# Kernel tuning notes

Hardware: AMD Instinct MI355X
Metric: run time of the kernel (lower is better)

## Reference

```python
import jax, jax.numpy as jnp
import numpy as np

EPS = 1e-5

def _quant_w(w):
    # symmetric per-tensor 8-bit weight quantization with straight-through estimator
    s = jnp.max(jnp.abs(w)) / 127.0
    wq = jnp.round(jnp.clip(w / s, -127.0, 127.0)) * s
    return w + jax.lax.stop_gradient(wq - w)

def _adder_conv(x, w, stride):
    # AdderNet conv: out[b,co,ow] = -sum_{cin,k} |x[b,cin,ow*stride+k] - w[co,cin,k]|
    # x: (B, Cin, L), w: (Co, Cin, K)
    B, Cin, L = x.shape
    Co, _, K = w.shape
    Ow = (L - K) // stride + 1
    idx = jnp.arange(Ow)[:, None] * stride + jnp.arange(K)[None, :]      # (Ow, K)
    patches = x[:, :, idx]                                               # (B, Cin, Ow, K)
    diff = jnp.abs(patches[:, None] - w[None, :, :, None, :])            # (B, Co, Cin, Ow, K)
    return -diff.sum(axis=(2, 4))                                        # (B, Co, Ow)

def _bn(x, p):
    # eval-mode BatchNorm; x: (B,C,W), p: (4,C) = [gamma, beta, running_mean, running_var]
    g, b, m, v = p
    return (x - m[:, None]) * (g[:, None] * jax.lax.rsqrt(v[:, None] + EPS)) + b[:, None]

def _bn_params(key, c):
    k1, k2, k3, k4 = jax.random.split(key, 4)
    g = jax.random.uniform(k1, (c,)) + 0.5
    b = 0.1 * jax.random.normal(k2, (c,))
    m = 0.1 * jax.random.normal(k3, (c,))
    v = jax.random.uniform(k4, (c,)) + 0.5
    return jnp.stack([g, b, m, v]).astype(jnp.float32)

def setup_inputs() -> dict:
    key = jax.random.key(0)
    ks = jax.random.split(key, 22)
    B = 8192
    w = lambda k, shp: (0.1 * jax.random.normal(k, shp)).astype(jnp.float32)
    return {
        'x': jax.random.normal(ks[0], (B, 1, 1, 256), dtype=jnp.float32),
        'w_pre1': w(ks[1], (5, 1, 13)),   'bn_pre1': _bn_params(ks[2], 5),
        'w_pre2': w(ks[3], (10, 5, 9)),   'bn_pre2': _bn_params(ks[4], 10),
        'w_r1':   w(ks[5], (10, 10, 1)),  'bn_r1':   _bn_params(ks[6], 10),
        'w_r2':   w(ks[7], (10, 10, 1)),  'bn_r2':   _bn_params(ks[8], 10),
        'w_o1a':  w(ks[9], (70, 140, 1)), 'bn_o1a':  _bn_params(ks[10], 70),
        'w_o1b':  w(ks[11], (30, 70, 1)), 'bn_o1b':  _bn_params(ks[12], 30),
        'w_o1c':  w(ks[13], (1, 30, 1)),  'bn_o1c':  _bn_params(ks[14], 1),
        'w_o2a':  w(ks[15], (70, 140, 1)),'bn_o2a':  _bn_params(ks[16], 70),
        'w_o2b':  w(ks[17], (30, 70, 1)), 'bn_o2b':  _bn_params(ks[18], 30),
        'w_o2c':  w(ks[19], (1, 30, 1)),  'bn_o2c':  _bn_params(ks[20], 1),
    }

def reference(x, w_pre1, bn_pre1, w_pre2, bn_pre2, w_r1, bn_r1, w_r2, bn_r2,
              w_o1a, bn_o1a, w_o1b, bn_o1b, w_o1c, bn_o1c,
              w_o2a, bn_o2a, w_o2b, bn_o2b, w_o2c, bn_o2c):
    relu = jax.nn.relu
    B = x.shape[0]
    h = x.reshape(B, 1, 256)                                  # height dim is 1 -> 1D
    h = relu(_bn(_adder_conv(h, _quant_w(w_pre1), 5), bn_pre1))   # (B,5,49)
    h = relu(_bn(_adder_conv(h, _quant_w(w_pre2), 3), bn_pre2))   # (B,10,14)
    # ResBlock
    t = relu(_bn(_adder_conv(h, _quant_w(w_r1), 1), bn_r1))
    t = _bn(_adder_conv(t, _quant_w(w_r2), 1), bn_r2)
    h = relu(t + h)                                           # (B,10,14)
    f = h.reshape(B, 140, 1)                                  # flatten to channels
    # O1 branch (amplitude-weighted average lifetime)
    a = relu(_bn(_adder_conv(f, _quant_w(w_o1a), 1), bn_o1a))
    a = relu(_bn(_adder_conv(a, _quant_w(w_o1b), 1), bn_o1b))
    a = relu(_bn(_adder_conv(a, _quant_w(w_o1c), 1), bn_o1c))
    tau_amp = a.reshape(-1)                                   # (B,)
    # O2 branch (intensity-weighted average lifetime)
    b = relu(_bn(_adder_conv(f, _quant_w(w_o2a), 1), bn_o2a))
    b = relu(_bn(_adder_conv(b, _quant_w(w_o2b), 1), bn_o2b))
    b = relu(_bn(_adder_conv(b, _quant_w(w_o2c), 1), bn_o2c))
    tau_inten = b.reshape(-1)                                 # (B,)
    return (tau_amp, tau_inten)
```

## Files before the change

### kernel.cpp

```cpp
#include <hip/hip_runtime.h>

#define TPB 256
#define EPB 8
#define H1S 246
#define ES  280

#define WQ1   0
#define WQ2   65
#define WR1Q  515
#define WR2Q  615
#define WCQ   715
#define WSB   779
#define SMALL_N 1253
#define WQAT  1280
#define WQBT  20880

#define SB_P1 0
#define SB_P2 10
#define SB_R1 30
#define SB_R2 50
#define SB_A1 70
#define SB_B1 210
#define SB_C1 270
#define SB_A2 272
#define SB_B2 412
#define SB_C2 472

#define GFOLD(bn, C, OFF)                                                     \
  if (tid < (C)) {                                                            \
    float gg = (bn)[tid], bb = (bn)[(C) + tid];                               \
    float mm = (bn)[2 * (C) + tid], vv = (bn)[3 * (C) + tid];                 \
    float sc = gg / sqrtf(vv + 1e-5f);                                        \
    sbp[(OFF) + tid] = sc;                                                    \
    sbp[(OFF) + (C) + tid] = bb - mm * sc;                                    \
  }

extern "C" __global__ __launch_bounds__(256)
void prep(const float* __restrict__ w1,  const float* __restrict__ bnp1,
          const float* __restrict__ w2,  const float* __restrict__ bnp2,
          const float* __restrict__ wr1, const float* __restrict__ bnr1,
          const float* __restrict__ wr2, const float* __restrict__ bnr2,
          const float* __restrict__ wa1, const float* __restrict__ bna1,
          const float* __restrict__ wb1, const float* __restrict__ bnb1,
          const float* __restrict__ wc1, const float* __restrict__ bnc1,
          const float* __restrict__ wa2, const float* __restrict__ bna2,
          const float* __restrict__ wb2, const float* __restrict__ bnb2,
          const float* __restrict__ wc2, const float* __restrict__ bnc2,
          float* __restrict__ ws)
{
  __shared__ float s_red[4];
  const int tid = threadIdx.x;
  const int b = blockIdx.x;

  if (b == 10) {
    float* sbp = ws + WSB;
    GFOLD(bnp1, 5, SB_P1)  GFOLD(bnp2, 10, SB_P2)
    GFOLD(bnr1, 10, SB_R1) GFOLD(bnr2, 10, SB_R2)
    GFOLD(bna1, 70, SB_A1) GFOLD(bnb1, 30, SB_B1) GFOLD(bnc1, 1, SB_C1)
    GFOLD(bna2, 70, SB_A2) GFOLD(bnb2, 30, SB_B2) GFOLD(bnc2, 1, SB_C2)
    return;
  }

  const float* src; int n; int mode; int rofs; float* dst = ws;
  int ofs = 0;
  switch (b) {
    case 0: src = w1;  ofs = WQ1;      n = 65;   mode = 0; rofs = 0;  break;
    case 1: src = w2;  ofs = WQ2;      n = 450;  mode = 0; rofs = 0;  break;
    case 2: src = wr1; ofs = WR1Q;     n = 100;  mode = 0; rofs = 0;  break;
    case 3: src = wr2; ofs = WR2Q;     n = 100;  mode = 0; rofs = 0;  break;
    case 4: src = wa1; ofs = WQAT;     n = 9800; mode = 1; rofs = 0;  break;
    case 5: src = wb1; ofs = WQBT;     n = 2100; mode = 2; rofs = 0;  break;
    case 6: src = wc1; ofs = WCQ;      n = 30;   mode = 0; rofs = 0;  break;
    case 7: src = wa2; ofs = WQAT;     n = 9800; mode = 1; rofs = 70; break;
    case 8: src = wb2; ofs = WQBT;     n = 2100; mode = 2; rofs = 30; break;
    default:src = wc2; ofs = WCQ + 32; n = 30;   mode = 0; rofs = 0;  break;
  }

  float m = 0.f;
  for (int i = tid; i < n; i += 256) m = fmaxf(m, fabsf(src[i]));
#pragma unroll
  for (int off = 32; off > 0; off >>= 1)
    m = fmaxf(m, __shfl_down(m, off, 64));
  if ((tid & 63) == 0) s_red[tid >> 6] = m;
  __syncthreads();
  m = fmaxf(fmaxf(s_red[0], s_red[1]), fmaxf(s_red[2], s_red[3]));

  float s = m / 127.0f;
  for (int i = tid; i < n; i += 256) {
    float w = src[i];
    float q = rintf(fminf(fmaxf(w / s, -127.f), 127.f)) * s;
    if (mode == 0) {
      dst[ofs + i] = q;
    } else if (mode == 1) {
      int r = i / 140 + rofs, c = i % 140;
      dst[ofs + ((c >> 2) * 140 + r) * 4 + (c & 3)] = q;
    } else {
      int r = i / 70 + rofs, c = i % 70;
      dst[ofs + ((c >> 1) * 60 + r) * 2 + (c & 1)] = q;
    }
  }
}

extern "C" __global__ __launch_bounds__(TPB, 4)
void taunet(const float* __restrict__ x, const float* __restrict__ ws,
            float* __restrict__ out, int B)
{
  __shared__ __align__(16) float s_h1[EPB * H1S];
  __shared__ __align__(16) float s_e[EPB * ES];
  __shared__ __align__(16) float s_small[SMALL_N];

  const int tid = threadIdx.x;
  const int g  = tid >> 5;
  const int l  = tid & 31;
  const int ln = tid & 63;
  const int wv = tid >> 6;
  const int gp = 2 * wv;
  const int elem = blockIdx.x * EPB + g;

  for (int i = WCQ + ln; i < SMALL_N; i += 64) s_small[i] = ws[i];

  {
    const float4* xb = (const float4*)x;
#pragma unroll
    for (int it = 0; it < 2; ++it) {
      int e = gp + it;
      int ge = blockIdx.x * EPB + e;
      if (ge < B) {
        float4 v = xb[ge * 64 + ln];
        *(float4*)&s_e[e * ES + ln * 4] = v;
      }
    }
  }

  {
    const float* xe = &s_e[g * ES];
#pragma unroll
    for (int rep = 0; rep < 2; ++rep) {
      int p = l + 32 * rep;
      bool act = p < 49;
      int ps = act ? p : 0;
      float win[13];
#pragma unroll
      for (int k = 0; k < 13; ++k) win[k] = xe[5 * ps + k];
#pragma unroll
      for (int ci = 0; ci < 5; ++ci) {
        float a0 = 0.f, a1 = 0.f;
#pragma unroll
        for (int k = 0; k < 13; ++k) {
          float d = fabsf(win[k] - ws[WQ1 + ci * 13 + k]);
          if (k & 1) a1 += d; else a0 += d;
        }
        float v = fmaxf(fmaf(-(a0 + a1), ws[WSB + SB_P1 + ci],
                             ws[WSB + SB_P1 + 5 + ci]), 0.f);
        if (act) s_h1[g * H1S + ci * 49 + ps] = v;
      }
    }
  }

  float h2r[10];
  {
    const bool act = l < 14;
    const int ow = act ? l : 0;
    const float* h1b = &s_h1[g * H1S];
    float acc[10] = {0.f,0.f,0.f,0.f,0.f,0.f,0.f,0.f,0.f,0.f};
#pragma unroll
    for (int ci = 0; ci < 5; ++ci) {
      float w9[9];
#pragma unroll
      for (int k = 0; k < 9; ++k) w9[k] = h1b[ci * 49 + 3 * ow + k];
#pragma unroll
      for (int co = 0; co < 10; ++co) {
        float s0 = 0.f, s1 = 0.f;
#pragma unroll
        for (int k = 0; k < 9; ++k) {
          float d = fabsf(w9[k] - ws[WQ2 + co * 45 + ci * 9 + k]);
          if (k & 1) s1 += d; else s0 += d;
        }
        acc[co] += s0 + s1;
      }
    }
#pragma unroll
    for (int co = 0; co < 10; ++co)
      h2r[co] = fmaxf(fmaf(-acc[co], ws[WSB + SB_P2 + co],
                           ws[WSB + SB_P2 + 10 + co]), 0.f);
  }

  float t1r[10];
#pragma unroll
  for (int co = 0; co < 10; ++co) {
    float a0 = 0.f, a1 = 0.f;
#pragma unroll
    for (int ci = 0; ci < 10; ++ci) {
      float d = fabsf(h2r[ci] - ws[WR1Q + co * 10 + ci]);
      if (ci & 1) a1 += d; else a0 += d;
    }
    t1r[co] = fmaxf(fmaf(-(a0 + a1), ws[WSB + SB_R1 + co],
                         ws[WSB + SB_R1 + 10 + co]), 0.f);
  }

#pragma unroll
  for (int co = 0; co < 10; ++co) {
    float a0 = 0.f, a1 = 0.f;
#pragma unroll
    for (int ci = 0; ci < 10; ++ci) {
      float d = fabsf(t1r[ci] - ws[WR2Q + co * 10 + ci]);
      if (ci & 1) a1 += d; else a0 += d;
    }
    float t2 = fmaf(-(a0 + a1), ws[WSB + SB_R2 + co], ws[WSB + SB_R2 + 10 + co]);
    float h = fmaxf(t2 + h2r[co], 0.f);
    if (l < 14) s_e[g * ES + co * 14 + l] = h;
  }

  {
    const float* hb0 = &s_e[gp * ES];
    const float* hb1 = &s_e[(gp + 1) * ES];

    const int r2 = (ln + 128 > 139) ? 139 : ln + 128;
    float accA[3][4], accB[3][4];
#pragma unroll
    for (int p = 0; p < 3; ++p)
#pragma unroll
      for (int j = 0; j < 4; ++j) { accA[p][j] = 0.f; accB[p][j] = 0.f; }
    const int rows[3] = {ln, ln + 64, r2};
#pragma unroll 2
    for (int cb = 0; cb < 35; ++cb) {
      float4 h4 = *(const float4*)&hb0[cb * 4];
      float4 k4 = *(const float4*)&hb1[cb * 4];
#pragma unroll
      for (int p = 0; p < 3; ++p) {
        float4 w4 = *(const float4*)&ws[WQAT + (cb * 140 + rows[p]) * 4];
        accA[p][0] += fabsf(h4.x - w4.x);
        accA[p][1] += fabsf(h4.y - w4.y);
        accA[p][2] += fabsf(h4.z - w4.z);
        accA[p][3] += fabsf(h4.w - w4.w);
        accB[p][0] += fabsf(k4.x - w4.x);
        accB[p][1] += fabsf(k4.y - w4.y);
        accB[p][2] += fabsf(k4.z - w4.z);
        accB[p][3] += fabsf(k4.w - w4.w);
      }
    }
#pragma unroll
    for (int p = 0; p < 3; ++p) {
      int cl = rows[p];
      bool act = (p < 2) || (ln < 12);
      if (act) {
        int co  = cl < 70 ? cl : cl - 70;
        int off = cl < 70 ? SB_A1 : SB_A2;
        float sc = s_small[WSB + off + co], bi = s_small[WSB + off + 70 + co];
        float sadA = (accA[p][0] + accA[p][1]) + (accA[p][2] + accA[p][3]);
        float sadB = (accB[p][0] + accB[p][1]) + (accB[p][2] + accB[p][3]);
        s_h1[gp * H1S + cl]       = fmaxf(fmaf(-sadA, sc, bi), 0.f);
        s_h1[(gp + 1) * H1S + cl] = fmaxf(fmaf(-sadB, sc, bi), 0.f);
      }
    }

    {
      bool act = ln < 60;
      int rl = act ? ln : 0;
      int br = rl >= 30;
      int co = br ? rl - 30 : rl;
      const float* h0 = &s_h1[gp * H1S + br * 70];
      const float* h1 = &s_h1[(gp + 1) * H1S + br * 70];
      int off = br ? SB_B2 : SB_B1;
      float a0 = 0.f, a1 = 0.f, b0 = 0.f, b1 = 0.f;
#pragma unroll 8
      for (int ci = 0; ci < 35; ++ci) {
        float2 w2v = *(const float2*)&ws[WQBT + (ci * 60 + rl) * 2];
        a0 += fabsf(h0[2 * ci]     - w2v.x);
        a1 += fabsf(h0[2 * ci + 1] - w2v.y);
        b0 += fabsf(h1[2 * ci]     - w2v.x);
        b1 += fabsf(h1[2 * ci + 1] - w2v.y);
      }
      if (act) {
        float sc = s_small[WSB + off + co], bi = s_small[WSB + off + 30 + co];
        s_e[gp * ES + 140 + rl]       = fmaxf(fmaf(-(a0 + a1), sc, bi), 0.f);
        s_e[(gp + 1) * ES + 140 + rl] = fmaxf(fmaf(-(b0 + b1), sc, bi), 0.f);
      }
    }

    for (int br = 0; br < 2; ++br) {
      float d = 0.f;
      if (l < 30)
        d = fabsf(s_e[g * ES + 140 + br * 30 + l] - s_small[WCQ + br * 32 + l]);
#pragma unroll
      for (int off = 16; off > 0; off >>= 1)
        d += __shfl_down(d, off, 32);
      if (l == 0 && elem < B) {
        int sbC = br ? SB_C2 : SB_C1;
        out[br * B + elem] =
            fmaxf(fmaf(-d, ws[WSB + sbC], ws[WSB + sbC + 1]), 0.f);
      }
    }
  }
}

extern "C" void kernel_launch(void* const* d_in, const int* in_sizes, int n_in,
                              void* d_out, int out_size, void* d_ws, size_t ws_size,
                              hipStream_t stream) {
  const float* x    = (const float*)d_in[0];
  const float* w1   = (const float*)d_in[1];
  const float* bnp1 = (const float*)d_in[2];
  const float* w2   = (const float*)d_in[3];
  const float* bnp2 = (const float*)d_in[4];
  const float* wr1  = (const float*)d_in[5];
  const float* bnr1 = (const float*)d_in[6];
  const float* wr2  = (const float*)d_in[7];
  const float* bnr2 = (const float*)d_in[8];
  const float* wa1  = (const float*)d_in[9];
  const float* bna1 = (const float*)d_in[10];
  const float* wb1  = (const float*)d_in[11];
  const float* bnb1 = (const float*)d_in[12];
  const float* wc1  = (const float*)d_in[13];
  const float* bnc1 = (const float*)d_in[14];
  const float* wa2  = (const float*)d_in[15];
  const float* bna2 = (const float*)d_in[16];
  const float* wb2  = (const float*)d_in[17];
  const float* bnb2 = (const float*)d_in[18];
  const float* wc2  = (const float*)d_in[19];
  const float* bnc2 = (const float*)d_in[20];

  float* ws = (float*)d_ws;
  int B = in_sizes[0] / 256;
  int blocks = (B + EPB - 1) / EPB;

  hipLaunchKernelGGL(prep, dim3(11), dim3(256), 0, stream,
                     w1, bnp1, w2, bnp2, wr1, bnr1, wr2, bnr2,
                     wa1, bna1, wb1, bnb1, wc1, bnc1,
                     wa2, bna2, wb2, bnb2, wc2, bnc2, ws);

  hipLaunchKernelGGL(taunet, dim3(blocks), dim3(TPB), 0, stream,
                     x, ws, (float*)d_out, B);
}
```

Measured before the change: 146.3 us.

## Process four elements per wavefront to reuse weight loads across more samples

The block now handles 16 samples instead of 8, and each 64-lane wavefront owns 4 samples instead of 2. The 140->70 and 70->30 adder layers reuse each global weight load across four samples rather than two, and the first layers are remapped to full 64-lane wavefronts. This aims to halve weight-load traffic per sample and cut grid size, at the cost of higher register use (48 accumulators) and more shared memory per block, which may reduce occupancy.

Result: no change. 148.4 us (+1.4%).

```diff
diff --git a/kernel.cpp b/kernel.cpp
--- a/kernel.cpp
+++ b/kernel.cpp
@@ -1,7 +1,7 @@
 #include <hip/hip_runtime.h>
 
 #define TPB 256
-#define EPB 8
+#define EPB 16
 #define H1S 246
 #define ES  280
 
@@ -110,58 +110,56 @@
   __shared__ __align__(16) float s_small[SMALL_N];
 
   const int tid = threadIdx.x;
-  const int g  = tid >> 5;
-  const int l  = tid & 31;
-  const int ln = tid & 63;
+  const int l  = tid & 63;
   const int wv = tid >> 6;
-  const int gp = 2 * wv;
-  const int elem = blockIdx.x * EPB + g;
-
-  for (int i = WCQ + ln; i < SMALL_N; i += 64) s_small[i] = ws[i];
+  const int gp = 4 * wv;
+  const int ebase = blockIdx.x * EPB + gp;
+
+  for (int i = WCQ + l; i < SMALL_N; i += 64) s_small[i] = ws[i];
 
   {
     const float4* xb = (const float4*)x;
 #pragma unroll
-    for (int it = 0; it < 2; ++it) {
-      int e = gp + it;
-      int ge = blockIdx.x * EPB + e;
+    for (int j = 0; j < 4; ++j) {
+      int ge = ebase + j;
       if (ge < B) {
-        float4 v = xb[ge * 64 + ln];
-        *(float4*)&s_e[e * ES + ln * 4] = v;
-      }
-    }
-  }
-
-  {
-    const float* xe = &s_e[g * ES];
-#pragma unroll
-    for (int rep = 0; rep < 2; ++rep) {
-      int p = l + 32 * rep;
-      bool act = p < 49;
-      int ps = act ? p : 0;
-      float win[13];
-#pragma unroll
-      for (int k = 0; k < 13; ++k) win[k] = xe[5 * ps + k];
-#pragma unroll
-      for (int ci = 0; ci < 5; ++ci) {
-        float a0 = 0.f, a1 = 0.f;
-#pragma unroll
-        for (int k = 0; k < 13; ++k) {
-          float d = fabsf(win[k] - ws[WQ1 + ci * 13 + k]);
-          if (k & 1) a1 += d; else a0 += d;
-        }
-        float v = fmaxf(fmaf(-(a0 + a1), ws[WSB + SB_P1 + ci],
-                             ws[WSB + SB_P1 + 5 + ci]), 0.f);
-        if (act) s_h1[g * H1S + ci * 49 + ps] = v;
-      }
-    }
-  }
+        float4 v = xb[ge * 64 + l];
+        *(float4*)&s_e[(gp + j) * ES + l * 4] = v;
+      }
+    }
+  }
+
+#pragma unroll
+  for (int j = 0; j < 4; ++j) {
+    const float* xe = &s_e[(gp + j) * ES];
+    bool act = l < 49;
+    int ps = act ? l : 0;
+    float win[13];
+#pragma unroll
+    for (int k = 0; k < 13; ++k) win[k] = xe[5 * ps + k];
+#pragma unroll
+    for (int ci = 0; ci < 5; ++ci) {
+      float a0 = 0.f, a1 = 0.f;
+#pragma unroll
+      for (int k = 0; k < 13; ++k) {
+        float d = fabsf(win[k] - ws[WQ1 + ci * 13 + k]);
+        if (k & 1) a1 += d; else a0 += d;
+      }
+      float v = fmaxf(fmaf(-(a0 + a1), ws[WSB + SB_P1 + ci],
+                           ws[WSB + SB_P1 + 5 + ci]), 0.f);
+      if (act) s_h1[(gp + j) * H1S + ci * 49 + ps] = v;
+    }
+  }
+
+  const int eloc = l >> 4;
+  const int slot = gp + eloc;
+  const int ow16 = l & 15;
+  const bool act = ow16 < 14;
+  const int ow = act ? ow16 : 0;
 
   float h2r[10];
   {
-    const bool act = l < 14;
-    const int ow = act ? l : 0;
-    const float* h1b = &s_h1[g * H1S];
+    const float* h1b = &s_h1[slot * H1S];
     float acc[10] = {0.f,0.f,0.f,0.f,0.f,0.f,0.f,0.f,0.f,0.f};
 #pragma unroll
     for (int ci = 0; ci < 5; ++ci) {
@@ -208,88 +206,97 @@
     }
     float t2 = fmaf(-(a0 + a1), ws[WSB + SB_R2 + co], ws[WSB + SB_R2 + 10 + co]);
     float h = fmaxf(t2 + h2r[co], 0.f);
-    if (l < 14) s_e[g * ES + co * 14 + l] = h;
+    if (act) s_e[slot * ES + co * 14 + ow] = h;
   }
 
   {
-    const float* hb0 = &s_e[gp * ES];
-    const float* hb1 = &s_e[(gp + 1) * ES];
-
-    const int r2 = (ln + 128 > 139) ? 139 : ln + 128;
-    float accA[3][4], accB[3][4];
+    const int r2 = (l + 128 > 139) ? 139 : l + 128;
+    const int rows[3] = {l, l + 64, r2};
+    float acc[3][4][4];
 #pragma unroll
     for (int p = 0; p < 3; ++p)
 #pragma unroll
-      for (int j = 0; j < 4; ++j) { accA[p][j] = 0.f; accB[p][j] = 0.f; }
-    const int rows[3] = {ln, ln + 64, r2};
-#pragma unroll 2
+      for (int e = 0; e < 4; ++e)
+#pragma unroll
+        for (int c = 0; c < 4; ++c) acc[p][e][c] = 0.f;
+#pragma unroll 1
     for (int cb = 0; cb < 35; ++cb) {
-      float4 h4 = *(const float4*)&hb0[cb * 4];
-      float4 k4 = *(const float4*)&hb1[cb * 4];
+      float4 h4[4];
+#pragma unroll
+      for (int e = 0; e < 4; ++e)
+        h4[e] = *(const float4*)&s_e[(gp + e) * ES + cb * 4];
 #pragma unroll
       for (int p = 0; p < 3; ++p) {
         float4 w4 = *(const float4*)&ws[WQAT + (cb * 140 + rows[p]) * 4];
-        accA[p][0] += fabsf(h4.x - w4.x);
-        accA[p][1] += fabsf(h4.y - w4.y);
-        accA[p][2] += fabsf(h4.z - w4.z);
-        accA[p][3] += fabsf(h4.w - w4.w);
-        accB[p][0] += fabsf(k4.x - w4.x);
-        accB[p][1] += fabsf(k4.y - w4.y);
-        accB[p][2] += fabsf(k4.z - w4.z);
-        accB[p][3] += fabsf(k4.w - w4.w);
+#pragma unroll
+        for (int e = 0; e < 4; ++e) {
+          acc[p][e][0] += fabsf(h4[e].x - w4.x);
+          acc[p][e][1] += fabsf(h4[e].y - w4.y);
+          acc[p][e][2] += fabsf(h4[e].z - w4.z);
+          acc[p][e][3] += fabsf(h4[e].w - w4.w);
+        }
       }
     }
 #pragma unroll
     for (int p = 0; p < 3; ++p) {
       int cl = rows[p];
-      bool act = (p < 2) || (ln < 12);
-      if (act) {
+      bool pact = (p < 2) || (l < 12);
+      if (pact) {
         int co  = cl < 70 ? cl : cl - 70;
         int off = cl < 70 ? SB_A1 : SB_A2;
         float sc = s_small[WSB + off + co], bi = s_small[WSB + off + 70 + co];
-        float sadA = (accA[p][0] + accA[p][1]) + (accA[p][2] + accA[p][3]);
-        float sadB = (accB[p][0] + accB[p][1]) + (accB[p][2] + accB[p][3]);
-        s_h1[gp * H1S + cl]       = fmaxf(fmaf(-sadA, sc, bi), 0.f);
-        s_h1[(gp + 1) * H1S + cl] = fmaxf(fmaf(-sadB, sc, bi), 0.f);
-      }
-    }
-
-    {
-      bool act = ln < 60;
-      int rl = act ? ln : 0;
-      int br = rl >= 30;
-      int co = br ? rl - 30 : rl;
-      const float* h0 = &s_h1[gp * H1S + br * 70];
-      const float* h1 = &s_h1[(gp + 1) * H1S + br * 70];
-      int off = br ? SB_B2 : SB_B1;
-      float a0 = 0.f, a1 = 0.f, b0 = 0.f, b1 = 0.f;
-#pragma unroll 8
-      for (int ci = 0; ci < 35; ++ci) {
-        float2 w2v = *(const float2*)&ws[WQBT + (ci * 60 + rl) * 2];
-        a0 += fabsf(h0[2 * ci]     - w2v.x);
-        a1 += fabsf(h0[2 * ci + 1] - w2v.y);
-        b0 += fabsf(h1[2 * ci]     - w2v.x);
-        b1 += fabsf(h1[2 * ci + 1] - w2v.y);
-      }
-      if (act) {
-        float sc = s_small[WSB + off + co], bi = s_small[WSB + off + 30 + co];
-        s_e[gp * ES + 140 + rl]       = fmaxf(fmaf(-(a0 + a1), sc, bi), 0.f);
-        s_e[(gp + 1) * ES + 140 + rl] = fmaxf(fmaf(-(b0 + b1), sc, bi), 0.f);
-      }
-    }
-
-    for (int br = 0; br < 2; ++br) {
-      float d = 0.f;
-      if (l < 30)
-        d = fabsf(s_e[g * ES + 140 + br * 30 + l] - s_small[WCQ + br * 32 + l]);
-#pragma unroll
-      for (int off = 16; off > 0; off >>= 1)
-        d += __shfl_down(d, off, 32);
-      if (l == 0 && elem < B) {
-        int sbC = br ? SB_C2 : SB_C1;
-        out[br * B + elem] =
-            fmaxf(fmaf(-d, ws[WSB + sbC], ws[WSB + sbC + 1]), 0.f);
-      }
+#pragma unroll
+        for (int e = 0; e < 4; ++e) {
+          float sad = (acc[p][e][0] + acc[p][e][1]) + (acc[p][e][2] + acc[p][e][3]);
+          s_h1[(gp + e) * H1S + cl] = fmaxf(fmaf(-sad, sc, bi), 0.f);
+        }
+      }
+    }
+  }
+
+  {
+    bool bact = l < 60;
+    int rl = bact ? l : 0;
+    int br = rl >= 30;
+    int co = br ? rl - 30 : rl;
+    int off = br ? SB_B2 : SB_B1;
+    float a0[4], a1[4];
+#pragma unroll
+    for (int e = 0; e < 4; ++e) { a0[e] = 0.f; a1[e] = 0.f; }
+#pragma unroll 4
+    for (int ci = 0; ci < 35; ++ci) {
+      float2 w2v = *(const float2*)&ws[WQBT + (ci * 60 + rl) * 2];
+#pragma unroll
+      for (int e = 0; e < 4; ++e) {
+        float2 h2 = *(const float2*)&s_h1[(gp + e) * H1S + br * 70 + 2 * ci];
+        a0[e] += fabsf(h2.x - w2v.x);
+        a1[e] += fabsf(h2.y - w2v.y);
+      }
+    }
+    if (bact) {
+      float sc = s_small[WSB + off + co], bi = s_small[WSB + off + 30 + co];
+#pragma unroll
+      for (int e = 0; e < 4; ++e)
+        s_e[(gp + e) * ES + 140 + rl] =
+            fmaxf(fmaf(-(a0[e] + a1[e]), sc, bi), 0.f);
+    }
+  }
+
+#pragma unroll
+  for (int j = 0; j < 4; ++j) {
+    int hw = l >> 5;
+    int i  = l & 31;
+    float d = 0.f;
+    if (i < 30)
+      d = fabsf(s_e[(gp + j) * ES + 140 + hw * 30 + i] -
+                s_small[WCQ + hw * 32 + i]);
+#pragma unroll
+    for (int off = 16; off > 0; off >>= 1)
+      d += __shfl_down(d, off, 32);
+    if (i == 0 && (ebase + j) < B) {
+      int sbC = hw ? SB_C2 : SB_C1;
+      out[hw * B + (ebase + j)] =
+          fmaxf(fmaf(-d, ws[WSB + sbC], ws[WSB + sbC + 1]), 0.f);
     }
   }
 }
```
